# Kernel tuning notes

Measured on AMD Instinct MI355X. Metric: run time of the kernel, lower is better.

The kernel has to match this reference:

```python
import jax, jax.numpy as jnp
import numpy as np
from functools import partial

NPOINT, NSAMPLE = 1024, 32
EPS = 1e-5

def setup_inputs() -> dict:
    key = jax.random.key(0)
    ks = jax.random.split(key, 16)
    B, N, C = 16, 4096, 64
    d = {
        "xyz": jax.random.normal(ks[0], (B, N, 3), jnp.float32),
        "points": jax.random.normal(ks[1], (B, N, C), jnp.float32),
    }
    chans = [67, 64, 64, 128]
    for i in range(3):
        cin, cout = chans[i], chans[i + 1]
        d[f"w{i+1}"] = jax.random.normal(ks[2 + i], (cout, cin), jnp.float32) * (1.0 / np.sqrt(cin))
        d[f"b{i+1}"] = jnp.zeros((cout,), jnp.float32)
        d[f"g{i+1}"] = jnp.ones((cout,), jnp.float32)
        d[f"be{i+1}"] = jnp.zeros((cout,), jnp.float32)
    return d

def farthest_point_sample(xyz, npoint):
    # xyz: (B, N, 3); deterministic start index 0 (torch code uses randint)
    B, N, _ = xyz.shape
    bidx = jnp.arange(B)

    def step(carry, _):
        distance, farthest = carry
        centroid = xyz[bidx, farthest]                       # (B, 3)
        dist = jnp.sum((xyz - centroid[:, None, :]) ** 2, -1)  # (B, N)
        distance = jnp.minimum(distance, dist)
        return (distance, jnp.argmax(distance, axis=1)), farthest

    init = (jnp.full((B, N), 1e10, xyz.dtype), jnp.zeros((B,), jnp.int32))
    _, centroids = jax.lax.scan(step, init, None, length=npoint)  # (npoint, B)
    return centroids.T                                            # (B, npoint)

def knn_group(nsample, xyz, new_xyz, points):
    # xyz: (B,N,3), new_xyz: (B,S,3), points: (B,N,C)
    # squared distances (same topk ordering as cdist)
    d2 = (jnp.sum(new_xyz ** 2, -1)[:, :, None]
          + jnp.sum(xyz ** 2, -1)[:, None, :]
          - 2.0 * jnp.einsum("bsd,bnd->bsn", new_xyz, xyz))     # (B,S,N)
    _, idx = jax.lax.top_k(-d2, nsample)                          # (B,S,K)

    gather = jax.vmap(lambda feats, i: feats[i])                  # per-batch fancy index
    grouped_xyz = gather(xyz, idx) - new_xyz[:, :, None, :]       # (B,S,K,3)
    grouped_pts = jnp.concatenate([grouped_xyz, gather(points, idx)], -1)  # (B,S,K,3+C)
    return grouped_xyz, grouped_pts

def mlp_layer(x, w, b, g, be):
    # 1x1 conv + BatchNorm (batch stats, training mode) + ReLU
    y = jnp.einsum("bskc,oc->bsko", x, w) + b
    mu = jnp.mean(y, axis=(0, 1, 2))
    var = jnp.var(y, axis=(0, 1, 2))
    y = (y - mu) * jax.lax.rsqrt(var + EPS) * g + be
    return jax.nn.relu(y)

def reference(xyz, points, w1, b1, g1, be1, w2, b2, g2, be2, w3, b3, g3, be3):
    centroids = farthest_point_sample(xyz, NPOINT)                    # (B,S)
    new_xyz = jnp.take_along_axis(xyz, centroids[:, :, None], axis=1)  # (B,S,3)
    _, x = knn_group(NSAMPLE, xyz, new_xyz, points)                   # (B,S,K,3+C)
    x = mlp_layer(x, w1, b1, g1, be1)
    x = mlp_layer(x, w2, b2, g2, be2)
    x = mlp_layer(x, w3, b3, g3, be3)
    new_points = jnp.max(x, axis=2)                                   # (B,S,mlp[-1])
    return new_xyz, new_points
```

## Files before the change

kernel.cpp:

```cpp
#include <hip/hip_runtime.h>

typedef unsigned int   uint;
typedef unsigned short ushort;
typedef unsigned long long u64;
typedef float f32x4 __attribute__((ext_vector_type(4)));

__device__ __forceinline__ void dot16x2(const float* __restrict__ wr,
                                        const f32x4* xa, const f32x4* xb,
                                        float& accA, float& accB){
#pragma unroll
  for (int k=0;k<4;k++){
    f32x4 w=*(const f32x4*)(wr+4*k);
    accA=fmaf(xa[k][0],w[0],accA); accA=fmaf(xa[k][1],w[1],accA);
    accA=fmaf(xa[k][2],w[2],accA); accA=fmaf(xa[k][3],w[3],accA);
    accB=fmaf(xb[k][0],w[0],accB); accB=fmaf(xb[k][1],w[1],accB);
    accB=fmaf(xb[k][2],w[2],accB); accB=fmaf(xb[k][3],w[3],accB);
  }
}

__global__ __launch_bounds__(256) void k_fps(const float* __restrict__ xyz,
                                             int* __restrict__ cent,
                                             float* __restrict__ oxyz){
  __shared__ __align__(16) float sp[4096][4];
  __shared__ u64 rk[2][4];
  __shared__ int sel[1024];
  const int b = blockIdx.x, tid = threadIdx.x, lane=tid&63, wave=tid>>6;
  const float* xb = xyz + (long)b*4096*3;
  float px[16], py[16], pz[16], pd[16];
#pragma unroll
  for (int j=0;j<16;j++){
    int n = tid + 256*j;
    float x=xb[n*3], y=xb[n*3+1], z=xb[n*3+2];
    sp[n][0]=x; sp[n][1]=y; sp[n][2]=z; sp[n][3]=0.0f;
    px[j]=x; py[j]=y; pz[j]=z; pd[j]=1e10f;
  }
  if (tid==0) sel[0]=0;
  __syncthreads();
  int f = 0;
  for (int t=1;t<1024;t++){
    f32x4 c = *(const f32x4*)sp[f];
    float bv=-1.0f; int bi=0;
#pragma unroll
    for (int j=0;j<16;j++){
      int n = tid + 256*j;
      float dx=px[j]-c[0], dy=py[j]-c[1], dz=pz[j]-c[2];
      float d=__fadd_rn(__fadd_rn(__fmul_rn(dx,dx),__fmul_rn(dy,dy)),__fmul_rn(dz,dz));
      float mn=fminf(pd[j],d); pd[j]=mn;
      if (j==0){ bv=mn; bi=n; }
      else if (mn>bv){ bv=mn; bi=n; }
    }
    u64 key = ((u64)__float_as_uint(bv)<<32) | (uint)(~bi);
#pragma unroll
    for (int off=32;off;off>>=1){
      u64 ok=__shfl_xor(key,off);
      key = ok>key ? ok : key;
    }
    int par=t&1;
    if (lane==0) rk[par][wave]=key;
    __syncthreads();
    {
      u64 k0=rk[par][0], k1=rk[par][1], k2=rk[par][2], k3=rk[par][3];
      u64 ka = k0>k1?k0:k1;
      u64 kb = k2>k3?k2:k3;
      u64 kk = ka>kb?ka:kb;
      f = (int)(~(uint)kk) & 4095;
    }
    if (tid==0) sel[t]=f;
  }
  __syncthreads();
#pragma unroll
  for (int j=0;j<4;j++){
    int s = tid + 256*j;
    int n = sel[s];
    cent[b*1024+s]=n;
    f32x4 cf=*(const f32x4*)sp[n];
    oxyz[(b*1024+s)*3+0]=cf[0];
    oxyz[(b*1024+s)*3+1]=cf[1];
    oxyz[(b*1024+s)*3+2]=cf[2];
  }
}

__global__ __launch_bounds__(256) void k_knn(const float* __restrict__ xyz,
                                             const int* __restrict__ cent,
                                             ushort* __restrict__ kidx){
  __shared__ float sx[4096], sy[4096], sz[4096];
  const int bx=blockIdx.x, b=bx>>5, chunk=bx&31;
  const int tid=threadIdx.x, lane=tid&63, wave=tid>>6;
  const float* xb = xyz + (long)b*4096*3;
#pragma unroll
  for (int j=0;j<16;j++){
    int n = tid + 256*j;
    sx[n]=xb[n*3]; sy[n]=xb[n*3+1]; sz[n]=xb[n*3+2];
  }
  __syncthreads();
  const u64 SENT=~0ull;
  for (int qp=0; qp<4; qp++){
    int sA = chunk*32 + wave*8 + qp*2;
    int sB = sA + 1;
    int qnA = cent[b*1024 + sA] & 4095;
    int qnB = cent[b*1024 + sB] & 4095;
    double qxA=(double)sx[qnA], qyA=(double)sy[qnA], qzA=(double)sz[qnA];
    double qxB=(double)sx[qnB], qyB=(double)sy[qnB], qzB=(double)sz[qnB];
    u64 k1A=SENT, k2A=SENT, k1B=SENT, k2B=SENT;
#pragma unroll 4
    for (int j=0;j<64;j++){
      int n = lane + 64*j;
      double px=(double)sx[n], py=(double)sy[n], pz=(double)sz[n];
      double dxA=px-qxA, dyA=py-qyA, dzA=pz-qzA;
      double dxB=px-qxB, dyB=py-qyB, dzB=pz-qzB;
      double d2A = dxA*dxA + dyA*dyA + dzA*dzA;
      double d2B = dxB*dxB + dyB*dyB + dzB*dzB;
      u64 kdA = (((u64)__double_as_longlong(d2A)) & ~4095ull) | (uint)n;
      u64 kdB = (((u64)__double_as_longlong(d2B)) & ~4095ull) | (uint)n;
      if (kdA<k1A){ k2A=k1A; k1A=kdA; }
      else if (kdA<k2A){ k2A=kdA; }
      if (kdB<k1B){ k2B=k1B; k1B=kdB; }
      else if (kdB<k2B){ k2B=kdB; }
    }
    u64 removedA=0ull, removedB=0ull;
    ushort* outA = kidx + (b*1024 + sA)*32;
    ushort* outB = kidx + (b*1024 + sB)*32;
    for (int r=0;r<32;r++){
      u64 wkA=k1A, wkB=k1B;
#pragma unroll
      for (int off=32;off;off>>=1){
        u64 okA=__shfl_xor(wkA,off);
        u64 okB=__shfl_xor(wkB,off);
        wkA = okA<wkA ? okA : wkA;
        wkB = okB<wkB ? okB : wkB;
      }
      if (lane==0){ outA[r]=(ushort)(wkA & 4095u); outB[r]=(ushort)(wkB & 4095u); }
      if (wkA==k1A){
        removedA |= 1ull << (((uint)(k1A&4095u))>>6);
        if (k2A!=SENT){ k1A=k2A; k2A=SENT; }
        else {
          k1A=SENT; k2A=SENT;
#pragma unroll 4
          for (int j=0;j<64;j++){
            if ((removedA>>j)&1ull) continue;
            int n = lane + 64*j;
            double dx=(double)sx[n]-qxA, dy=(double)sy[n]-qyA, dz=(double)sz[n]-qzA;
            double d2 = dx*dx + dy*dy + dz*dz;
            u64 kd = (((u64)__double_as_longlong(d2)) & ~4095ull) | (uint)n;
            if (kd<k1A){ k2A=k1A; k1A=kd; }
            else if (kd<k2A){ k2A=kd; }
          }
        }
      }
      if (wkB==k1B){
        removedB |= 1ull << (((uint)(k1B&4095u))>>6);
        if (k2B!=SENT){ k1B=k2B; k2B=SENT; }
        else {
          k1B=SENT; k2B=SENT;
#pragma unroll 4
          for (int j=0;j<64;j++){
            if ((removedB>>j)&1ull) continue;
            int n = lane + 64*j;
            double dx=(double)sx[n]-qxB, dy=(double)sy[n]-qyB, dz=(double)sz[n]-qzB;
            double d2 = dx*dx + dy*dy + dz*dz;
            u64 kd = (((u64)__double_as_longlong(d2)) & ~4095ull) | (uint)n;
            if (kd<k1B){ k2B=k1B; k1B=kd; }
            else if (kd<k2B){ k2B=kd; }
          }
        }
      }
    }
  }
}

__global__ __launch_bounds__(256) void k_mlp1b(const float* __restrict__ xyz,
                                               const float* __restrict__ pts,
                                               const float* __restrict__ w1,
                                               const float* __restrict__ b1,
                                               const int* __restrict__ cent,
                                               const ushort* __restrict__ kidx,
                                               float* __restrict__ part,
                                               float* __restrict__ y){
  __shared__ __align__(16) float L[9760];
  float* W1  = L;
  float* XIN = L+4384;
  float* WRED= L+8736;
  const int tid=threadIdx.x, bi=blockIdx.x;
  const int row=tid>>3, oc=tid&7, wave=tid>>6;
  const int b=bi>>6, s0=(bi&63)*16;
  const long bN=(long)b*4096;

  for (int i=tid;i<64*68;i+=256){
    int r=i/68, c=i-r*68;
    float v = (c<64)? w1[r*67+3+c] : (c<67? w1[r*67+(c-64)] : 0.0f);
    W1[r*68+((r>>3)<<2)+c]=v;
  }
  float breg1[8];
#pragma unroll
  for (int i=0;i<8;i++) breg1[i]=b1[oc*8+i];
  float ps[8], pq[8];
#pragma unroll
  for (int s=0;s<8;s++){ ps[s]=0.f; pq[s]=0.f; }
  __syncthreads();

  for (int t=0; t<8; t++){
    int sgA = b*1024 + s0 + t*2, sgB = sgA+1;
    {
      int nA = kidx[sgA*32+row] & 4095;
      int nB = kidx[sgB*32+row] & 4095;
      const float* prA = pts + (bN+nA)*64;
      const float* prB = pts + (bN+nB)*64;
      *(f32x4*)(XIN + row*68 + oc*8)          = *(const f32x4*)(prA + oc*8);
      *(f32x4*)(XIN + row*68 + oc*8 + 4)      = *(const f32x4*)(prA + oc*8 + 4);
      *(f32x4*)(XIN + (row+32)*68 + oc*8)     = *(const f32x4*)(prB + oc*8);
      *(f32x4*)(XIN + (row+32)*68 + oc*8 + 4) = *(const f32x4*)(prB + oc*8 + 4);
      if (oc==0){
        int qA = cent[sgA] & 4095, qB = cent[sgB] & 4095;
        const float* xpA = xyz + (bN+nA)*3; const float* qpA = xyz + (bN+qA)*3;
        const float* xpB = xyz + (bN+nB)*3; const float* qpB = xyz + (bN+qB)*3;
        XIN[row*68+64]=xpA[0]-qpA[0]; XIN[row*68+65]=xpA[1]-qpA[1];
        XIN[row*68+66]=xpA[2]-qpA[2]; XIN[row*68+67]=0.0f;
        XIN[(row+32)*68+64]=xpB[0]-qpB[0]; XIN[(row+32)*68+65]=xpB[1]-qpB[1];
        XIN[(row+32)*68+66]=xpB[2]-qpB[2]; XIN[(row+32)*68+67]=0.0f;
      }
    }
    const float* xrowA = XIN + row*68;
    const float* xrowB = XIN + (row+32)*68;
    float acc[2][8];
#pragma unroll
    for (int i=0;i<8;i++){ acc[0][i]=breg1[i]; acc[1][i]=breg1[i]; }
#pragma unroll
    for (int co=0;co<4;co++){
      f32x4 xa[4], xbv[4];
#pragma unroll
      for (int k=0;k<4;k++){ xa[k]=*(const f32x4*)(xrowA+co*16+4*k); xbv[k]=*(const f32x4*)(xrowB+co*16+4*k); }
#pragma unroll
      for (int i=0;i<8;i++)
        dot16x2(W1+(oc*8+i)*68+(oc<<2)+co*16, xa, xbv, acc[0][i], acc[1][i]);
    }
    {
      f32x4 xtA=*(const f32x4*)(xrowA+64), xtB=*(const f32x4*)(xrowB+64);
#pragma unroll
      for (int i=0;i<8;i++){
        const float* wr=W1+(oc*8+i)*68+(oc<<2)+64;
        f32x4 w=*(const f32x4*)wr;
        acc[0][i]=fmaf(xtA[0],w[0],acc[0][i]); acc[0][i]=fmaf(xtA[1],w[1],acc[0][i]);
        acc[0][i]=fmaf(xtA[2],w[2],acc[0][i]); acc[0][i]=fmaf(xtA[3],w[3],acc[0][i]);
        acc[1][i]=fmaf(xtB[0],w[0],acc[1][i]); acc[1][i]=fmaf(xtB[1],w[1],acc[1][i]);
        acc[1][i]=fmaf(xtB[2],w[2],acc[1][i]); acc[1][i]=fmaf(xtB[3],w[3],acc[1][i]);
      }
    }
    {
      long baseA = ((long)sgA*32+row)*64 + oc*8;
      long baseB = ((long)sgB*32+row)*64 + oc*8;
      *(f32x4*)(y+baseA)   = (f32x4){acc[0][0],acc[0][1],acc[0][2],acc[0][3]};
      *(f32x4*)(y+baseA+4) = (f32x4){acc[0][4],acc[0][5],acc[0][6],acc[0][7]};
      *(f32x4*)(y+baseB)   = (f32x4){acc[1][0],acc[1][1],acc[1][2],acc[1][3]};
      *(f32x4*)(y+baseB+4) = (f32x4){acc[1][4],acc[1][5],acc[1][6],acc[1][7]};
    }
#pragma unroll
    for (int i=0;i<8;i++){
      ps[i]+=acc[0][i]+acc[1][i];
      pq[i]=fmaf(acc[0][i],acc[0][i],pq[i]); pq[i]=fmaf(acc[1][i],acc[1][i],pq[i]);
    }
  }
#pragma unroll
  for (int s=0;s<8;s++){
    ps[s]+=__shfl_xor(ps[s],8); ps[s]+=__shfl_xor(ps[s],16); ps[s]+=__shfl_xor(ps[s],32);
    pq[s]+=__shfl_xor(pq[s],8); pq[s]+=__shfl_xor(pq[s],16); pq[s]+=__shfl_xor(pq[s],32);
  }
  __syncthreads();
  if ((tid&63)<8){
    for (int s=0;s<8;s++){
      WRED[((wave*8+oc)*16+s)*2+0]=ps[s];
      WRED[((wave*8+oc)*16+s)*2+1]=pq[s];
    }
  }
  __syncthreads();
  if (tid<64){
    int o=tid, occ=o>>3, i=o&7;
    float s=0.f,q=0.f;
#pragma unroll
    for (int w=0;w<4;w++){ s+=WRED[((w*8+occ)*16+i)*2]; q+=WRED[((w*8+occ)*16+i)*2+1]; }
    part[(bi*64+o)*2]=s; part[(bi*64+o)*2+1]=q;
  }
}

__global__ __launch_bounds__(256) void k_mlp2b(const float* __restrict__ w2,
                                               const float* __restrict__ b2,
                                               const float* __restrict__ ab1,
                                               float* __restrict__ part,
                                               float* __restrict__ y){
  __shared__ __align__(16) float L[9504];
  float* W2  = L;
  float* XIN = L+4128;
  float* WRED= L+8480;
  const int tid=threadIdx.x, bi=blockIdx.x;
  const int row=tid>>3, oc=tid&7, wave=tid>>6;
  const int b=bi>>6, s0=(bi&63)*16;

  for (int i=tid;i<4096;i+=256){
    int r=i>>6, c=i&63;
    W2[r*64+((r>>3)<<2)+c]=w2[i];
  }
  float areg1[8],creg1[8],breg2[8];
#pragma unroll
  for (int i=0;i<8;i++){ int ch=oc*8+i; areg1[i]=ab1[ch*2]; creg1[i]=ab1[ch*2+1]; breg2[i]=b2[ch]; }
  float ps[8], pq[8];
#pragma unroll
  for (int s=0;s<8;s++){ ps[s]=0.f; pq[s]=0.f; }
  __syncthreads();

  for (int t=0; t<8; t++){
    int sgA = b*1024 + s0 + t*2, sgB = sgA+1;
    long baseA = ((long)sgA*32+row)*64 + oc*8;
    long baseB = ((long)sgB*32+row)*64 + oc*8;
    {
      f32x4 ya0=*(const f32x4*)(y+baseA), ya1=*(const f32x4*)(y+baseA+4);
      f32x4 yb0=*(const f32x4*)(y+baseB), yb1=*(const f32x4*)(y+baseB+4);
      f32x4 xo;
      xo[0]=fmaxf(fmaf(areg1[0],ya0[0],creg1[0]),0.0f);
      xo[1]=fmaxf(fmaf(areg1[1],ya0[1],creg1[1]),0.0f);
      xo[2]=fmaxf(fmaf(areg1[2],ya0[2],creg1[2]),0.0f);
      xo[3]=fmaxf(fmaf(areg1[3],ya0[3],creg1[3]),0.0f);
      *(f32x4*)(XIN+row*68+oc*8)=xo;
      xo[0]=fmaxf(fmaf(areg1[4],ya1[0],creg1[4]),0.0f);
      xo[1]=fmaxf(fmaf(areg1[5],ya1[1],creg1[5]),0.0f);
      xo[2]=fmaxf(fmaf(areg1[6],ya1[2],creg1[6]),0.0f);
      xo[3]=fmaxf(fmaf(areg1[7],ya1[3],creg1[7]),0.0f);
      *(f32x4*)(XIN+row*68+oc*8+4)=xo;
      xo[0]=fmaxf(fmaf(areg1[0],yb0[0],creg1[0]),0.0f);
      xo[1]=fmaxf(fmaf(areg1[1],yb0[1],creg1[1]),0.0f);
      xo[2]=fmaxf(fmaf(areg1[2],yb0[2],creg1[2]),0.0f);
      xo[3]=fmaxf(fmaf(areg1[3],yb0[3],creg1[3]),0.0f);
      *(f32x4*)(XIN+(row+32)*68+oc*8)=xo;
      xo[0]=fmaxf(fmaf(areg1[4],yb1[0],creg1[4]),0.0f);
      xo[1]=fmaxf(fmaf(areg1[5],yb1[1],creg1[5]),0.0f);
      xo[2]=fmaxf(fmaf(areg1[6],yb1[2],creg1[6]),0.0f);
      xo[3]=fmaxf(fmaf(areg1[7],yb1[3],creg1[7]),0.0f);
      *(f32x4*)(XIN+(row+32)*68+oc*8+4)=xo;
    }
    const float* x2A = XIN + row*68;
    const float* x2B = XIN + (row+32)*68;
    float acc2[2][8];
#pragma unroll
    for (int i=0;i<8;i++){ acc2[0][i]=breg2[i]; acc2[1][i]=breg2[i]; }
#pragma unroll
    for (int co=0;co<4;co++){
      f32x4 xa[4], xbv[4];
#pragma unroll
      for (int k=0;k<4;k++){ xa[k]=*(const f32x4*)(x2A+co*16+4*k); xbv[k]=*(const f32x4*)(x2B+co*16+4*k); }
#pragma unroll
      for (int i=0;i<8;i++)
        dot16x2(W2+(oc*8+i)*64+(oc<<2)+co*16, xa, xbv, acc2[0][i], acc2[1][i]);
    }
    *(f32x4*)(y+baseA)   = (f32x4){acc2[0][0],acc2[0][1],acc2[0][2],acc2[0][3]};
    *(f32x4*)(y+baseA+4) = (f32x4){acc2[0][4],acc2[0][5],acc2[0][6],acc2[0][7]};
    *(f32x4*)(y+baseB)   = (f32x4){acc2[1][0],acc2[1][1],acc2[1][2],acc2[1][3]};
    *(f32x4*)(y+baseB+4) = (f32x4){acc2[1][4],acc2[1][5],acc2[1][6],acc2[1][7]};
#pragma unroll
    for (int i=0;i<8;i++){
      ps[i]+=acc2[0][i]+acc2[1][i];
      pq[i]=fmaf(acc2[0][i],acc2[0][i],pq[i]); pq[i]=fmaf(acc2[1][i],acc2[1][i],pq[i]);
    }
  }
#pragma unroll
  for (int s=0;s<8;s++){
    ps[s]+=__shfl_xor(ps[s],8); ps[s]+=__shfl_xor(ps[s],16); ps[s]+=__shfl_xor(ps[s],32);
    pq[s]+=__shfl_xor(pq[s],8); pq[s]+=__shfl_xor(pq[s],16); pq[s]+=__shfl_xor(pq[s],32);
  }
  __syncthreads();
  if ((tid&63)<8){
    for (int s=0;s<8;s++){
      WRED[((wave*8+oc)*16+s)*2+0]=ps[s];
      WRED[((wave*8+oc)*16+s)*2+1]=pq[s];
    }
  }
  __syncthreads();
  if (tid<64){
    int o=tid, occ=o>>3, i=o&7;
    float s=0.f,q=0.f;
#pragma unroll
    for (int w=0;w<4;w++){ s+=WRED[((w*8+occ)*16+i)*2]; q+=WRED[((w*8+occ)*16+i)*2+1]; }
    part[(bi*64+o)*2]=s; part[(bi*64+o)*2+1]=q;
  }
}

__global__ __launch_bounds__(256) void k_mlp3b(const float* __restrict__ w3,
                                               const float* __restrict__ b3,
                                               const float* __restrict__ ab2,
                                               float* __restrict__ part,
                                               const float* __restrict__ y,
                                               float* __restrict__ mx){
  __shared__ __align__(16) float L[13696];
  float* W3F = L;
  float* XIN = L+8320;
  float* WRED= L+12672;
  const int tid=threadIdx.x, bi=blockIdx.x;
  const int row=tid>>3, oc=tid&7, wave=tid>>6;
  const int b=bi>>6, s0=(bi&63)*16;

  for (int i=tid;i<8192;i+=256){
    int og=i>>11, rem=i&2047, r=rem>>6, c=rem&63;
    W3F[og*2080 + r*64+((r>>2)<<2)+c]=w3[i];
  }
  float areg2[8],creg2[8];
#pragma unroll
  for (int i=0;i<8;i++){ int ch=oc*8+i; areg2[i]=ab2[ch*2]; creg2[i]=ab2[ch*2+1]; }
  float breg3[16];
#pragma unroll
  for (int og=0;og<4;og++)
#pragma unroll
    for (int i=0;i<4;i++) breg3[og*4+i]=b3[og*32+oc*4+i];
  float ps[16], pq[16];
#pragma unroll
  for (int s=0;s<16;s++){ ps[s]=0.f; pq[s]=0.f; }
  __syncthreads();

  for (int t=0; t<8; t++){
    int sgA = b*1024 + s0 + t*2, sgB = sgA+1;
    long baseA = ((long)sgA*32+row)*64 + oc*8;
    long baseB = ((long)sgB*32+row)*64 + oc*8;
    {
      f32x4 ya0=*(const f32x4*)(y+baseA), ya1=*(const f32x4*)(y+baseA+4);
      f32x4 yb0=*(const f32x4*)(y+baseB), yb1=*(const f32x4*)(y+baseB+4);
      f32x4 xo;
      xo[0]=fmaxf(fmaf(areg2[0],ya0[0],creg2[0]),0.0f);
      xo[1]=fmaxf(fmaf(areg2[1],ya0[1],creg2[1]),0.0f);
      xo[2]=fmaxf(fmaf(areg2[2],ya0[2],creg2[2]),0.0f);
      xo[3]=fmaxf(fmaf(areg2[3],ya0[3],creg2[3]),0.0f);
      *(f32x4*)(XIN+row*68+oc*8)=xo;
      xo[0]=fmaxf(fmaf(areg2[4],ya1[0],creg2[4]),0.0f);
      xo[1]=fmaxf(fmaf(areg2[5],ya1[1],creg2[5]),0.0f);
      xo[2]=fmaxf(fmaf(areg2[6],ya1[2],creg2[6]),0.0f);
      xo[3]=fmaxf(fmaf(areg2[7],ya1[3],creg2[7]),0.0f);
      *(f32x4*)(XIN+row*68+oc*8+4)=xo;
      xo[0]=fmaxf(fmaf(areg2[0],yb0[0],creg2[0]),0.0f);
      xo[1]=fmaxf(fmaf(areg2[1],yb0[1],creg2[1]),0.0f);
      xo[2]=fmaxf(fmaf(areg2[2],yb0[2],creg2[2]),0.0f);
      xo[3]=fmaxf(fmaf(areg2[3],yb0[3],creg2[3]),0.0f);
      *(f32x4*)(XIN+(row+32)*68+oc*8)=xo;
      xo[0]=fmaxf(fmaf(areg2[4],yb1[0],creg2[4]),0.0f);
      xo[1]=fmaxf(fmaf(areg2[5],yb1[1],creg2[5]),0.0f);
      xo[2]=fmaxf(fmaf(areg2[6],yb1[2],creg2[6]),0.0f);
      xo[3]=fmaxf(fmaf(areg2[7],yb1[3],creg2[7]),0.0f);
      *(f32x4*)(XIN+(row+32)*68+oc*8+4)=xo;
    }
    const float* x2A = XIN + row*68;
    const float* x2B = XIN + (row+32)*68;
    float acc3[4][2][4];
#pragma unroll
    for (int og=0;og<4;og++)
#pragma unroll
      for (int i=0;i<4;i++){ acc3[og][0][i]=breg3[og*4+i]; acc3[og][1][i]=breg3[og*4+i]; }
#pragma unroll
    for (int co=0;co<4;co++){
      f32x4 xa[4], xbv[4];
#pragma unroll
      for (int k=0;k<4;k++){ xa[k]=*(const f32x4*)(x2A+co*16+4*k); xbv[k]=*(const f32x4*)(x2B+co*16+4*k); }
#pragma unroll
      for (int og=0;og<4;og++)
#pragma unroll
        for (int i=0;i<4;i++)
          dot16x2(W3F+og*2080+(oc*4+i)*64+(oc<<2)+co*16, xa, xbv, acc3[og][0][i], acc3[og][1][i]);
    }
    float vm[2][16];
#pragma unroll
    for (int og=0;og<4;og++)
#pragma unroll
      for (int i=0;i<4;i++){
        int s=og*4+i;
        ps[s]+=acc3[og][0][i]+acc3[og][1][i];
        pq[s]=fmaf(acc3[og][0][i],acc3[og][0][i],pq[s]); pq[s]=fmaf(acc3[og][1][i],acc3[og][1][i],pq[s]);
        vm[0][s]=acc3[og][0][i]; vm[1][s]=acc3[og][1][i];
      }
    {
#pragma unroll
      for (int q=0;q<2;q++)
#pragma unroll
        for (int s=0;s<16;s++){
          vm[q][s]=fmaxf(vm[q][s],__shfl_xor(vm[q][s],8));
          vm[q][s]=fmaxf(vm[q][s],__shfl_xor(vm[q][s],16));
          vm[q][s]=fmaxf(vm[q][s],__shfl_xor(vm[q][s],32));
        }
      __syncthreads();
      if ((tid&63)<8){
#pragma unroll
        for (int q=0;q<2;q++)
#pragma unroll
          for (int s=0;s<16;s++) WRED[(q*32 + wave*8+oc)*16 + s]=vm[q][s];
      }
      __syncthreads();
      {
        int q=tid>>7, o=tid&127;
        int og=o>>5, occ=(o&31)>>2, s=og*4+(o&3);
        float v=WRED[(q*32 + 0*8+occ)*16+s];
        v=fmaxf(v,WRED[(q*32 + 1*8+occ)*16+s]);
        v=fmaxf(v,WRED[(q*32 + 2*8+occ)*16+s]);
        v=fmaxf(v,WRED[(q*32 + 3*8+occ)*16+s]);
        mx[(long)(q? sgB : sgA)*128+o]=v;
      }
    }
  }
  {
#pragma unroll
    for (int s=0;s<16;s++){
      ps[s]+=__shfl_xor(ps[s],8); ps[s]+=__shfl_xor(ps[s],16); ps[s]+=__shfl_xor(ps[s],32);
      pq[s]+=__shfl_xor(pq[s],8); pq[s]+=__shfl_xor(pq[s],16); pq[s]+=__shfl_xor(pq[s],32);
    }
    __syncthreads();
    if ((tid&63)<8){
      for (int s=0;s<16;s++){
        WRED[((wave*8+oc)*16+s)*2+0]=ps[s];
        WRED[((wave*8+oc)*16+s)*2+1]=pq[s];
      }
    }
    __syncthreads();
    if (tid<128){
      int o=tid, og=o>>5, occ=(o&31)>>2, i=o&3, s2=og*4+i;
      float s=0.f,q=0.f;
#pragma unroll
      for (int w=0;w<4;w++){ s+=WRED[((w*8+occ)*16+s2)*2]; q+=WRED[((w*8+occ)*16+s2)*2+1]; }
      part[(bi*128+o)*2]=s; part[(bi*128+o)*2+1]=q;
    }
  }
}

__global__ void k_red(const float* __restrict__ part,
                      const float* __restrict__ gam,
                      const float* __restrict__ bet,
                      float* __restrict__ ab, int nch, int nblk){
  __shared__ float red[4][128][2];
  const int tid=threadIdx.x, ch=tid%nch, seg=tid/nch;
  float s=0.f,q=0.f;
  for (int i=seg;i<nblk;i+=4){ s+=part[(i*nch+ch)*2]; q+=part[(i*nch+ch)*2+1]; }
  red[seg][ch][0]=s; red[seg][ch][1]=q;
  __syncthreads();
  if (seg==0){
    s=red[0][ch][0]+red[1][ch][0]+red[2][ch][0]+red[3][ch][0];
    q=red[0][ch][1]+red[1][ch][1]+red[2][ch][1]+red[3][ch][1];
    float mu=s*(1.0f/524288.0f);
    float var=q*(1.0f/524288.0f)-mu*mu;
    var=fmaxf(var,0.0f);
    float a=gam[ch]/sqrtf(var+1e-5f);
    float c=bet[ch]-mu*a;
    ab[ch*2]=a; ab[ch*2+1]=c;
  }
}

__global__ __launch_bounds__(256) void k_out(const float* __restrict__ mx,
                                             const float* __restrict__ ab3,
                                             float* __restrict__ onp){
  int i = (blockIdx.x*256 + threadIdx.x)*4;
  int ch = i & 127;
  f32x4 v = *(const f32x4*)(mx+i);
  f32x4 r;
  r[0]=fmaxf(fmaf(ab3[(ch+0)*2], v[0], ab3[(ch+0)*2+1]), 0.0f);
  r[1]=fmaxf(fmaf(ab3[(ch+1)*2], v[1], ab3[(ch+1)*2+1]), 0.0f);
  r[2]=fmaxf(fmaf(ab3[(ch+2)*2], v[2], ab3[(ch+2)*2+1]), 0.0f);
  r[3]=fmaxf(fmaf(ab3[(ch+3)*2], v[3], ab3[(ch+3)*2+1]), 0.0f);
  *(f32x4*)(onp+i)=r;
}

extern "C" void kernel_launch(void* const* d_in, const int* in_sizes, int n_in,
                              void* d_out, int out_size, void* d_ws, size_t ws_size,
                              hipStream_t stream){
  const float* xyz=(const float*)d_in[0];
  const float* pts=(const float*)d_in[1];
  const float* w1 =(const float*)d_in[2];
  const float* b1 =(const float*)d_in[3];
  const float* g1 =(const float*)d_in[4];
  const float* be1=(const float*)d_in[5];
  const float* w2 =(const float*)d_in[6];
  const float* b2 =(const float*)d_in[7];
  const float* g2 =(const float*)d_in[8];
  const float* be2=(const float*)d_in[9];
  const float* w3 =(const float*)d_in[10];
  const float* b3 =(const float*)d_in[11];
  const float* g3 =(const float*)d_in[12];
  const float* be3=(const float*)d_in[13];
  char* ws=(char*)d_ws;
  int*    cent=(int*)(ws);
  ushort* kidx=(ushort*)(ws+  65536);
  float*  p   =(float*)(ws+ 1114112);
  float*  ab1 =(float*)(ws+ 2162688);
  float*  ab2 =(float*)(ws+ 2163200);
  float*  ab3 =(float*)(ws+ 2163712);
  float*  mx  =(float*)(ws+ 2164736);
  float*  y   =(float*)(ws+16777216);
  float* oxyz=(float*)d_out;
  float* onp =oxyz + 16*1024*3;

  k_fps<<<16, 256, 0, stream>>>(xyz, cent, oxyz);
  k_knn<<<512, 256, 0, stream>>>(xyz, cent, kidx);
  k_mlp1b<<<1024, 256, 0, stream>>>(xyz, pts, w1, b1, cent, kidx, p, y);
  k_red<<<1, 256, 0, stream>>>(p, g1, be1, ab1, 64, 1024);
  k_mlp2b<<<1024, 256, 0, stream>>>(w2, b2, ab1, p, y);
  k_red<<<1, 256, 0, stream>>>(p, g2, be2, ab2, 64, 1024);
  k_mlp3b<<<1024, 256, 0, stream>>>(w3, b3, ab2, p, y, mx);
  k_red<<<1, 512, 0, stream>>>(p, g3, be3, ab3, 128, 1024);
  k_out<<<2048, 256, 0, stream>>>(mx, ab3, onp);
}
```

Measured before the change: 2.008 ms.

## Use bf16 MFMA for MLP layers 2 and 3 with smaller per-block tiles

Replaces the scalar FP32 FMA matmuls in the second and third MLP layers with bf16 MFMA 16x16x32 instructions. Activations and weights are converted to bf16 and staged in padded LDS tiles. Each block now handles 128 rows, so the grid grows to 4096 blocks and partial BN statistics go to a larger buffer reduced by k_red. Converting to bf16 lowers precision and may shift the BN statistics and max outputs.

```diff
diff --git a/kernel.cpp b/kernel.cpp
--- a/kernel.cpp
+++ b/kernel.cpp
@@ -4,6 +4,19 @@
 typedef unsigned short ushort;
 typedef unsigned long long u64;
 typedef float f32x4 __attribute__((ext_vector_type(4)));
+typedef short bf16x8 __attribute__((ext_vector_type(8)));
+typedef uint  uint2v __attribute__((ext_vector_type(2)));
+
+#define STR 88
+
+__device__ __forceinline__ uint packbf2(float a, float b){
+  uint ua=__float_as_uint(a); ua=(ua+0x7fffu+((ua>>16)&1u))>>16;
+  uint ub=__float_as_uint(b); ub=(ub+0x7fffu+((ub>>16)&1u))>>16;
+  return ua|(ub<<16);
+}
+__device__ __forceinline__ ushort bf1(float a){
+  uint ua=__float_as_uint(a); return (ushort)((ua+0x7fffu+((ua>>16)&1u))>>16);
+}
 
 __device__ __forceinline__ void dot16x2(const float* __restrict__ wr,
                                         const f32x4* xa, const f32x4* xb,
@@ -281,243 +294,198 @@
   }
 }
 
-__global__ __launch_bounds__(256) void k_mlp2b(const float* __restrict__ w2,
+
+__global__ __launch_bounds__(256) void k_mlp2m(const float* __restrict__ w2,
                                                const float* __restrict__ b2,
                                                const float* __restrict__ ab1,
                                                float* __restrict__ part,
                                                float* __restrict__ y){
-  __shared__ __align__(16) float L[9504];
-  float* W2  = L;
-  float* XIN = L+4128;
-  float* WRED= L+8480;
+  __shared__ __align__(16) ushort SA[128*STR];
+  __shared__ __align__(16) ushort SW[64*STR];
+  __shared__ float WRED[4*4*16*2];
   const int tid=threadIdx.x, bi=blockIdx.x;
-  const int row=tid>>3, oc=tid&7, wave=tid>>6;
-  const int b=bi>>6, s0=(bi&63)*16;
+  const int lane=tid&63, wave=tid>>6;
+  const int lo16=lane&15, hi16=lane>>4;
+  const long row0=(long)bi*128;
 
   for (int i=tid;i<4096;i+=256){
     int r=i>>6, c=i&63;
-    W2[r*64+((r>>3)<<2)+c]=w2[i];
-  }
-  float areg1[8],creg1[8],breg2[8];
-#pragma unroll
-  for (int i=0;i<8;i++){ int ch=oc*8+i; areg1[i]=ab1[ch*2]; creg1[i]=ab1[ch*2+1]; breg2[i]=b2[ch]; }
-  float ps[8], pq[8];
-#pragma unroll
-  for (int s=0;s<8;s++){ ps[s]=0.f; pq[s]=0.f; }
-  __syncthreads();
-
-  for (int t=0; t<8; t++){
-    int sgA = b*1024 + s0 + t*2, sgB = sgA+1;
-    long baseA = ((long)sgA*32+row)*64 + oc*8;
-    long baseB = ((long)sgB*32+row)*64 + oc*8;
-    {
-      f32x4 ya0=*(const f32x4*)(y+baseA), ya1=*(const f32x4*)(y+baseA+4);
-      f32x4 yb0=*(const f32x4*)(y+baseB), yb1=*(const f32x4*)(y+baseB+4);
-      f32x4 xo;
-      xo[0]=fmaxf(fmaf(areg1[0],ya0[0],creg1[0]),0.0f);
-      xo[1]=fmaxf(fmaf(areg1[1],ya0[1],creg1[1]),0.0f);
-      xo[2]=fmaxf(fmaf(areg1[2],ya0[2],creg1[2]),0.0f);
-      xo[3]=fmaxf(fmaf(areg1[3],ya0[3],creg1[3]),0.0f);
-      *(f32x4*)(XIN+row*68+oc*8)=xo;
-      xo[0]=fmaxf(fmaf(areg1[4],ya1[0],creg1[4]),0.0f);
-      xo[1]=fmaxf(fmaf(areg1[5],ya1[1],creg1[5]),0.0f);
-      xo[2]=fmaxf(fmaf(areg1[6],ya1[2],creg1[6]),0.0f);
-      xo[3]=fmaxf(fmaf(areg1[7],ya1[3],creg1[7]),0.0f);
-      *(f32x4*)(XIN+row*68+oc*8+4)=xo;
-      xo[0]=fmaxf(fmaf(areg1[0],yb0[0],creg1[0]),0.0f);
-      xo[1]=fmaxf(fmaf(areg1[1],yb0[1],creg1[1]),0.0f);
-      xo[2]=fmaxf(fmaf(areg1[2],yb0[2],creg1[2]),0.0f);
-      xo[3]=fmaxf(fmaf(areg1[3],yb0[3],creg1[3]),0.0f);
-      *(f32x4*)(XIN+(row+32)*68+oc*8)=xo;
-      xo[0]=fmaxf(fmaf(areg1[4],yb1[0],creg1[4]),0.0f);
-      xo[1]=fmaxf(fmaf(areg1[5],yb1[1],creg1[5]),0.0f);
-      xo[2]=fmaxf(fmaf(areg1[6],yb1[2],creg1[6]),0.0f);
-      xo[3]=fmaxf(fmaf(areg1[7],yb1[3],creg1[7]),0.0f);
-      *(f32x4*)(XIN+(row+32)*68+oc*8+4)=xo;
-    }
-    const float* x2A = XIN + row*68;
-    const float* x2B = XIN + (row+32)*68;
-    float acc2[2][8];
-#pragma unroll
-    for (int i=0;i<8;i++){ acc2[0][i]=breg2[i]; acc2[1][i]=breg2[i]; }
-#pragma unroll
-    for (int co=0;co<4;co++){
-      f32x4 xa[4], xbv[4];
-#pragma unroll
-      for (int k=0;k<4;k++){ xa[k]=*(const f32x4*)(x2A+co*16+4*k); xbv[k]=*(const f32x4*)(x2B+co*16+4*k); }
-#pragma unroll
-      for (int i=0;i<8;i++)
-        dot16x2(W2+(oc*8+i)*64+(oc<<2)+co*16, xa, xbv, acc2[0][i], acc2[1][i]);
-    }
-    *(f32x4*)(y+baseA)   = (f32x4){acc2[0][0],acc2[0][1],acc2[0][2],acc2[0][3]};
-    *(f32x4*)(y+baseA+4) = (f32x4){acc2[0][4],acc2[0][5],acc2[0][6],acc2[0][7]};
-    *(f32x4*)(y+baseB)   = (f32x4){acc2[1][0],acc2[1][1],acc2[1][2],acc2[1][3]};
-    *(f32x4*)(y+baseB+4) = (f32x4){acc2[1][4],acc2[1][5],acc2[1][6],acc2[1][7]};
-#pragma unroll
-    for (int i=0;i<8;i++){
-      ps[i]+=acc2[0][i]+acc2[1][i];
-      pq[i]=fmaf(acc2[0][i],acc2[0][i],pq[i]); pq[i]=fmaf(acc2[1][i],acc2[1][i],pq[i]);
-    }
-  }
-#pragma unroll
-  for (int s=0;s<8;s++){
-    ps[s]+=__shfl_xor(ps[s],8); ps[s]+=__shfl_xor(ps[s],16); ps[s]+=__shfl_xor(ps[s],32);
-    pq[s]+=__shfl_xor(pq[s],8); pq[s]+=__shfl_xor(pq[s],16); pq[s]+=__shfl_xor(pq[s],32);
-  }
-  __syncthreads();
-  if ((tid&63)<8){
-    for (int s=0;s<8;s++){
-      WRED[((wave*8+oc)*16+s)*2+0]=ps[s];
-      WRED[((wave*8+oc)*16+s)*2+1]=pq[s];
+    SW[r*STR+c]=bf1(w2[i]);
+  }
+  {
+    int ch4=(tid&15)*4;
+    float a1[4],c1[4];
+#pragma unroll
+    for(int j=0;j<4;j++){ a1[j]=ab1[(ch4+j)*2]; c1[j]=ab1[(ch4+j)*2+1]; }
+    int rb=(tid>>4)*8;
+#pragma unroll
+    for(int rr=0;rr<8;rr++){
+      int r=rb+rr;
+      f32x4 v=*(const f32x4*)(y+(row0+r)*64+ch4);
+      float x0=fmaxf(fmaf(a1[0],v[0],c1[0]),0.f);
+      float x1=fmaxf(fmaf(a1[1],v[1],c1[1]),0.f);
+      float x2=fmaxf(fmaf(a1[2],v[2],c1[2]),0.f);
+      float x3=fmaxf(fmaf(a1[3],v[3],c1[3]),0.f);
+      uint2v p; p[0]=packbf2(x0,x1); p[1]=packbf2(x2,x3);
+      *(uint2v*)(SA+r*STR+ch4)=p;
+    }
+  }
+  __syncthreads();
+
+  const int mt=wave*32;
+  f32x4 acc[2][4];
+#pragma unroll
+  for(int mf=0;mf<2;mf++)
+#pragma unroll
+    for(int nf=0;nf<4;nf++) acc[mf][nf]=(f32x4){0.f,0.f,0.f,0.f};
+#pragma unroll
+  for (int ks=0; ks<2; ks++){
+    bf16x8 a0=*(const bf16x8*)(SA+(mt+lo16)*STR    + ks*32 + hi16*8);
+    bf16x8 a1=*(const bf16x8*)(SA+(mt+16+lo16)*STR + ks*32 + hi16*8);
+    bf16x8 b0=*(const bf16x8*)(SW+(lo16)*STR     + ks*32 + hi16*8);
+    bf16x8 b1=*(const bf16x8*)(SW+(16+lo16)*STR  + ks*32 + hi16*8);
+    bf16x8 b2f=*(const bf16x8*)(SW+(32+lo16)*STR + ks*32 + hi16*8);
+    bf16x8 b3f=*(const bf16x8*)(SW+(48+lo16)*STR + ks*32 + hi16*8);
+    acc[0][0]=__builtin_amdgcn_mfma_f32_16x16x32_bf16(a0,b0 ,acc[0][0],0,0,0);
+    acc[0][1]=__builtin_amdgcn_mfma_f32_16x16x32_bf16(a0,b1 ,acc[0][1],0,0,0);
+    acc[0][2]=__builtin_amdgcn_mfma_f32_16x16x32_bf16(a0,b2f,acc[0][2],0,0,0);
+    acc[0][3]=__builtin_amdgcn_mfma_f32_16x16x32_bf16(a0,b3f,acc[0][3],0,0,0);
+    acc[1][0]=__builtin_amdgcn_mfma_f32_16x16x32_bf16(a1,b0 ,acc[1][0],0,0,0);
+    acc[1][1]=__builtin_amdgcn_mfma_f32_16x16x32_bf16(a1,b1 ,acc[1][1],0,0,0);
+    acc[1][2]=__builtin_amdgcn_mfma_f32_16x16x32_bf16(a1,b2f,acc[1][2],0,0,0);
+    acc[1][3]=__builtin_amdgcn_mfma_f32_16x16x32_bf16(a1,b3f,acc[1][3],0,0,0);
+  }
+  float pss[4]={0.f,0.f,0.f,0.f}, pqq[4]={0.f,0.f,0.f,0.f};
+#pragma unroll
+  for (int nf=0;nf<4;nf++){
+    float bb=b2[nf*16+lo16];
+#pragma unroll
+    for (int mf=0;mf<2;mf++)
+#pragma unroll
+      for (int reg=0;reg<4;reg++){
+        float d=acc[mf][nf][reg]+bb;
+        long rr=row0+mt+mf*16+hi16*4+reg;
+        y[rr*64 + nf*16+lo16]=d;
+        pss[nf]+=d; pqq[nf]=fmaf(d,d,pqq[nf]);
+      }
+  }
+#pragma unroll
+  for (int nf=0;nf<4;nf++){
+    pss[nf]+=__shfl_xor(pss[nf],16); pss[nf]+=__shfl_xor(pss[nf],32);
+    pqq[nf]+=__shfl_xor(pqq[nf],16); pqq[nf]+=__shfl_xor(pqq[nf],32);
+  }
+  if (lane<16){
+#pragma unroll
+    for (int nf=0;nf<4;nf++){
+      WRED[((wave*4+nf)*16+lane)*2+0]=pss[nf];
+      WRED[((wave*4+nf)*16+lane)*2+1]=pqq[nf];
     }
   }
   __syncthreads();
   if (tid<64){
-    int o=tid, occ=o>>3, i=o&7;
+    int ch=tid, nf=ch>>4, ci=ch&15;
     float s=0.f,q=0.f;
 #pragma unroll
-    for (int w=0;w<4;w++){ s+=WRED[((w*8+occ)*16+i)*2]; q+=WRED[((w*8+occ)*16+i)*2+1]; }
-    part[(bi*64+o)*2]=s; part[(bi*64+o)*2+1]=q;
-  }
-}
-
-__global__ __launch_bounds__(256) void k_mlp3b(const float* __restrict__ w3,
+    for (int w=0;w<4;w++){ s+=WRED[((w*4+nf)*16+ci)*2]; q+=WRED[((w*4+nf)*16+ci)*2+1]; }
+    part[(bi*64+ch)*2]=s; part[(bi*64+ch)*2+1]=q;
+  }
+}
+
+__global__ __launch_bounds__(256) void k_mlp3m(const float* __restrict__ w3,
                                                const float* __restrict__ b3,
                                                const float* __restrict__ ab2,
                                                float* __restrict__ part,
                                                const float* __restrict__ y,
                                                float* __restrict__ mx){
-  __shared__ __align__(16) float L[13696];
-  float* W3F = L;
-  float* XIN = L+8320;
-  float* WRED= L+12672;
+  __shared__ __align__(16) ushort SA[128*STR];
+  __shared__ __align__(16) ushort SW[128*STR];
+  __shared__ float WRED[4*8*16*2];
   const int tid=threadIdx.x, bi=blockIdx.x;
-  const int row=tid>>3, oc=tid&7, wave=tid>>6;
-  const int b=bi>>6, s0=(bi&63)*16;
+  const int lane=tid&63, wave=tid>>6;
+  const int lo16=lane&15, hi16=lane>>4;
+  const long row0=(long)bi*128;
 
   for (int i=tid;i<8192;i+=256){
-    int og=i>>11, rem=i&2047, r=rem>>6, c=rem&63;
-    W3F[og*2080 + r*64+((r>>2)<<2)+c]=w3[i];
-  }
-  float areg2[8],creg2[8];
-#pragma unroll
-  for (int i=0;i<8;i++){ int ch=oc*8+i; areg2[i]=ab2[ch*2]; creg2[i]=ab2[ch*2+1]; }
-  float breg3[16];
-#pragma unroll
-  for (int og=0;og<4;og++)
-#pragma unroll
-    for (int i=0;i<4;i++) breg3[og*4+i]=b3[og*32+oc*4+i];
-  float ps[16], pq[16];
-#pragma unroll
-  for (int s=0;s<16;s++){ ps[s]=0.f; pq[s]=0.f; }
-  __syncthreads();
-
-  for (int t=0; t<8; t++){
-    int sgA = b*1024 + s0 + t*2, sgB = sgA+1;
-    long baseA = ((long)sgA*32+row)*64 + oc*8;
-    long baseB = ((long)sgB*32+row)*64 + oc*8;
-    {
-      f32x4 ya0=*(const f32x4*)(y+baseA), ya1=*(const f32x4*)(y+baseA+4);
-      f32x4 yb0=*(const f32x4*)(y+baseB), yb1=*(const f32x4*)(y+baseB+4);
-      f32x4 xo;
-      xo[0]=fmaxf(fmaf(areg2[0],ya0[0],creg2[0]),0.0f);
-      xo[1]=fmaxf(fmaf(areg2[1],ya0[1],creg2[1]),0.0f);
-      xo[2]=fmaxf(fmaf(areg2[2],ya0[2],creg2[2]),0.0f);
-      xo[3]=fmaxf(fmaf(areg2[3],ya0[3],creg2[3]),0.0f);
-      *(f32x4*)(XIN+row*68+oc*8)=xo;
-      xo[0]=fmaxf(fmaf(areg2[4],ya1[0],creg2[4]),0.0f);
-      xo[1]=fmaxf(fmaf(areg2[5],ya1[1],creg2[5]),0.0f);
-      xo[2]=fmaxf(fmaf(areg2[6],ya1[2],creg2[6]),0.0f);
-      xo[3]=fmaxf(fmaf(areg2[7],ya1[3],creg2[7]),0.0f);
-      *(f32x4*)(XIN+row*68+oc*8+4)=xo;
-      xo[0]=fmaxf(fmaf(areg2[0],yb0[0],creg2[0]),0.0f);
-      xo[1]=fmaxf(fmaf(areg2[1],yb0[1],creg2[1]),0.0f);
-      xo[2]=fmaxf(fmaf(areg2[2],yb0[2],creg2[2]),0.0f);
-      xo[3]=fmaxf(fmaf(areg2[3],yb0[3],creg2[3]),0.0f);
-      *(f32x4*)(XIN+(row+32)*68+oc*8)=xo;
-      xo[0]=fmaxf(fmaf(areg2[4],yb1[0],creg2[4]),0.0f);
-      xo[1]=fmaxf(fmaf(areg2[5],yb1[1],creg2[5]),0.0f);
-      xo[2]=fmaxf(fmaf(areg2[6],yb1[2],creg2[6]),0.0f);
-      xo[3]=fmaxf(fmaf(areg2[7],yb1[3],creg2[7]),0.0f);
-      *(f32x4*)(XIN+(row+32)*68+oc*8+4)=xo;
-    }
-    const float* x2A = XIN + row*68;
-    const float* x2B = XIN + (row+32)*68;
-    float acc3[4][2][4];
-#pragma unroll
-    for (int og=0;og<4;og++)
-#pragma unroll
-      for (int i=0;i<4;i++){ acc3[og][0][i]=breg3[og*4+i]; acc3[og][1][i]=breg3[og*4+i]; }
-#pragma unroll
-    for (int co=0;co<4;co++){
-      f32x4 xa[4], xbv[4];
-#pragma unroll
-      for (int k=0;k<4;k++){ xa[k]=*(const f32x4*)(x2A+co*16+4*k); xbv[k]=*(const f32x4*)(x2B+co*16+4*k); }
-#pragma unroll
-      for (int og=0;og<4;og++)
-#pragma unroll
-        for (int i=0;i<4;i++)
-          dot16x2(W3F+og*2080+(oc*4+i)*64+(oc<<2)+co*16, xa, xbv, acc3[og][0][i], acc3[og][1][i]);
-    }
-    float vm[2][16];
-#pragma unroll
-    for (int og=0;og<4;og++)
-#pragma unroll
-      for (int i=0;i<4;i++){
-        int s=og*4+i;
-        ps[s]+=acc3[og][0][i]+acc3[og][1][i];
-        pq[s]=fmaf(acc3[og][0][i],acc3[og][0][i],pq[s]); pq[s]=fmaf(acc3[og][1][i],acc3[og][1][i],pq[s]);
-        vm[0][s]=acc3[og][0][i]; vm[1][s]=acc3[og][1][i];
-      }
-    {
-#pragma unroll
-      for (int q=0;q<2;q++)
-#pragma unroll
-        for (int s=0;s<16;s++){
-          vm[q][s]=fmaxf(vm[q][s],__shfl_xor(vm[q][s],8));
-          vm[q][s]=fmaxf(vm[q][s],__shfl_xor(vm[q][s],16));
-          vm[q][s]=fmaxf(vm[q][s],__shfl_xor(vm[q][s],32));
-        }
-      __syncthreads();
-      if ((tid&63)<8){
-#pragma unroll
-        for (int q=0;q<2;q++)
-#pragma unroll
-          for (int s=0;s<16;s++) WRED[(q*32 + wave*8+oc)*16 + s]=vm[q][s];
-      }
-      __syncthreads();
-      {
-        int q=tid>>7, o=tid&127;
-        int og=o>>5, occ=(o&31)>>2, s=og*4+(o&3);
-        float v=WRED[(q*32 + 0*8+occ)*16+s];
-        v=fmaxf(v,WRED[(q*32 + 1*8+occ)*16+s]);
-        v=fmaxf(v,WRED[(q*32 + 2*8+occ)*16+s]);
-        v=fmaxf(v,WRED[(q*32 + 3*8+occ)*16+s]);
-        mx[(long)(q? sgB : sgA)*128+o]=v;
-      }
-    }
+    int r=i>>6, c=i&63;
+    SW[r*STR+c]=bf1(w3[i]);
   }
   {
-#pragma unroll
-    for (int s=0;s<16;s++){
-      ps[s]+=__shfl_xor(ps[s],8); ps[s]+=__shfl_xor(ps[s],16); ps[s]+=__shfl_xor(ps[s],32);
-      pq[s]+=__shfl_xor(pq[s],8); pq[s]+=__shfl_xor(pq[s],16); pq[s]+=__shfl_xor(pq[s],32);
-    }
-    __syncthreads();
-    if ((tid&63)<8){
-      for (int s=0;s<16;s++){
-        WRED[((wave*8+oc)*16+s)*2+0]=ps[s];
-        WRED[((wave*8+oc)*16+s)*2+1]=pq[s];
-      }
-    }
-    __syncthreads();
-    if (tid<128){
-      int o=tid, og=o>>5, occ=(o&31)>>2, i=o&3, s2=og*4+i;
-      float s=0.f,q=0.f;
-#pragma unroll
-      for (int w=0;w<4;w++){ s+=WRED[((w*8+occ)*16+s2)*2]; q+=WRED[((w*8+occ)*16+s2)*2+1]; }
-      part[(bi*128+o)*2]=s; part[(bi*128+o)*2+1]=q;
-    }
+    int ch4=(tid&15)*4;
+    float a2[4],c2[4];
+#pragma unroll
+    for(int j=0;j<4;j++){ a2[j]=ab2[(ch4+j)*2]; c2[j]=ab2[(ch4+j)*2+1]; }
+    int rb=(tid>>4)*8;
+#pragma unroll
+    for(int rr=0;rr<8;rr++){
+      int r=rb+rr;
+      f32x4 v=*(const f32x4*)(y+(row0+r)*64+ch4);
+      float x0=fmaxf(fmaf(a2[0],v[0],c2[0]),0.f);
+      float x1=fmaxf(fmaf(a2[1],v[1],c2[1]),0.f);
+      float x2=fmaxf(fmaf(a2[2],v[2],c2[2]),0.f);
+      float x3=fmaxf(fmaf(a2[3],v[3],c2[3]),0.f);
+      uint2v p; p[0]=packbf2(x0,x1); p[1]=packbf2(x2,x3);
+      *(uint2v*)(SA+r*STR+ch4)=p;
+    }
+  }
+  __syncthreads();
+
+  const int mt=wave*32;
+  f32x4 acc[2][8];
+#pragma unroll
+  for(int mf=0;mf<2;mf++)
+#pragma unroll
+    for(int nf=0;nf<8;nf++) acc[mf][nf]=(f32x4){0.f,0.f,0.f,0.f};
+#pragma unroll
+  for (int ks=0; ks<2; ks++){
+    bf16x8 a0=*(const bf16x8*)(SA+(mt+lo16)*STR    + ks*32 + hi16*8);
+    bf16x8 a1=*(const bf16x8*)(SA+(mt+16+lo16)*STR + ks*32 + hi16*8);
+#pragma unroll
+    for (int nf=0;nf<8;nf++){
+      bf16x8 bv=*(const bf16x8*)(SW+(nf*16+lo16)*STR + ks*32 + hi16*8);
+      acc[0][nf]=__builtin_amdgcn_mfma_f32_16x16x32_bf16(a0,bv,acc[0][nf],0,0,0);
+      acc[1][nf]=__builtin_amdgcn_mfma_f32_16x16x32_bf16(a1,bv,acc[1][nf],0,0,0);
+    }
+  }
+  float pss[8], pqq[8], vmx[8];
+#pragma unroll
+  for (int nf=0;nf<8;nf++){ pss[nf]=0.f; pqq[nf]=0.f; vmx[nf]=-3.0e38f; }
+#pragma unroll
+  for (int nf=0;nf<8;nf++){
+    float bb=b3[nf*16+lo16];
+#pragma unroll
+    for (int mf=0;mf<2;mf++)
+#pragma unroll
+      for (int reg=0;reg<4;reg++){
+        float d=acc[mf][nf][reg]+bb;
+        pss[nf]+=d; pqq[nf]=fmaf(d,d,pqq[nf]);
+        vmx[nf]=fmaxf(vmx[nf],d);
+      }
+  }
+#pragma unroll
+  for (int nf=0;nf<8;nf++){
+    pss[nf]+=__shfl_xor(pss[nf],16); pss[nf]+=__shfl_xor(pss[nf],32);
+    pqq[nf]+=__shfl_xor(pqq[nf],16); pqq[nf]+=__shfl_xor(pqq[nf],32);
+    vmx[nf]=fmaxf(vmx[nf],__shfl_xor(vmx[nf],16));
+    vmx[nf]=fmaxf(vmx[nf],__shfl_xor(vmx[nf],32));
+  }
+  {
+    long sg = (row0>>5) + wave;
+    if (lane<16){
+#pragma unroll
+      for (int nf=0;nf<8;nf++){
+        mx[sg*128 + nf*16 + lane]=vmx[nf];
+        WRED[((wave*8+nf)*16+lane)*2+0]=pss[nf];
+        WRED[((wave*8+nf)*16+lane)*2+1]=pqq[nf];
+      }
+    }
+  }
+  __syncthreads();
+  if (tid<128){
+    int ch=tid, nf=ch>>4, ci=ch&15;
+    float s=0.f,q=0.f;
+#pragma unroll
+    for (int w=0;w<4;w++){ s+=WRED[((w*8+nf)*16+ci)*2]; q+=WRED[((w*8+nf)*16+ci)*2+1]; }
+    part[(bi*128+ch)*2]=s; part[(bi*128+ch)*2+1]=q;
   }
 }
 
@@ -582,6 +550,7 @@
   float*  ab2 =(float*)(ws+ 2163200);
   float*  ab3 =(float*)(ws+ 2163712);
   float*  mx  =(float*)(ws+ 2164736);
+  float*  pb  =(float*)(ws+11534336);
   float*  y   =(float*)(ws+16777216);
   float* oxyz=(float*)d_out;
   float* onp =oxyz + 16*1024*3;
@@ -590,9 +559,9 @@
   k_knn<<<512, 256, 0, stream>>>(xyz, cent, kidx);
   k_mlp1b<<<1024, 256, 0, stream>>>(xyz, pts, w1, b1, cent, kidx, p, y);
   k_red<<<1, 256, 0, stream>>>(p, g1, be1, ab1, 64, 1024);
-  k_mlp2b<<<1024, 256, 0, stream>>>(w2, b2, ab1, p, y);
-  k_red<<<1, 256, 0, stream>>>(p, g2, be2, ab2, 64, 1024);
-  k_mlp3b<<<1024, 256, 0, stream>>>(w3, b3, ab2, p, y, mx);
-  k_red<<<1, 512, 0, stream>>>(p, g3, be3, ab3, 128, 1024);
+  k_mlp2m<<<4096, 256, 0, stream>>>(w2, b2, ab1, pb, y);
+  k_red<<<1, 256, 0, stream>>>(pb, g2, be2, ab2, 64, 4096);
+  k_mlp3m<<<4096, 256, 0, stream>>>(w3, b3, ab2, pb, y, mx);
+  k_red<<<1, 512, 0, stream>>>(pb, g3, be3, ab3, 128, 4096);
   k_out<<<2048, 256, 0, stream>>>(mx, ab3, onp);
 }
```

After: 2.151 ms. +7.1%, slower.
